# Optimization experiments

Hardware: AMD Instinct MI355X
Metric: run time of the kernel (lower is better)

## Reference

```python
import jax, jax.numpy as jnp
import numpy as np

N_ATOMS = 200_000
N_EDGES = 10_000_000
N_MOL = 128


def setup_inputs() -> dict:
    key = jax.random.key(0)
    k1, k2, k3, k4, k5, k6, k7 = jax.random.split(key, 7)
    dEdRij = jax.random.normal(k1, (N_EDGES, 3), dtype=jnp.float32)
    Rij = jax.random.normal(k2, (N_EDGES, 3), dtype=jnp.float32)
    R = jax.random.normal(k3, (N_ATOMS, 3), dtype=jnp.float32)
    # Non-degenerate cells: ~10 Angstrom cubic boxes with small perturbation
    cell = jnp.eye(3, dtype=jnp.float32) * 10.0 + 0.1 * jax.random.normal(k4, (N_MOL, 3, 3), dtype=jnp.float32)
    idx_i = jax.random.randint(k5, (N_EDGES,), 0, N_ATOMS, dtype=jnp.int32)
    idx_j = jax.random.randint(k6, (N_EDGES,), 0, N_ATOMS, dtype=jnp.int32)
    idx_m = jnp.sort(jax.random.randint(k7, (N_ATOMS,), 0, N_MOL, dtype=jnp.int32))
    return {"dEdRij": dEdRij, "Rij": Rij, "R": R, "cell": cell,
            "idx_i": idx_i, "idx_j": idx_j, "idx_m": idx_m}


def reference(dEdRij, Rij, R, cell, idx_i, idx_j, idx_m):
    N = R.shape[0]
    M = cell.shape[0]
    # Forces: F = sum_{edges into i} dE/dRij - sum_{edges from j} dE/dRij
    forces = jnp.zeros_like(R).at[idx_i].add(dEdRij).at[idx_j].add(-dEdRij)
    # Per-edge outer product [E,3,3]: Rij[:, :, None] * dEdRij[:, None, :]
    stress_edge = dEdRij[:, None, :] * Rij[:, :, None]
    # Scatter to atoms, then reduce atoms -> molecules
    stress_i = jnp.zeros((N, 3, 3), dtype=R.dtype).at[idx_i].add(stress_edge)
    stress = jax.ops.segment_sum(stress_i, idx_m, num_segments=M)  # [M,3,3]
    # Cell volume via scalar triple product a . (b x c)
    volume = jnp.sum(cell[:, 0, :] * jnp.cross(cell[:, 1, :], cell[:, 2, :]), axis=1)  # [M]
    stress_out = (stress / volume[:, None, None]).reshape(M * 3, 3)
    return forces, stress_out
```

## Files before the change

### kernel.cpp

```cpp
#include <hip/hip_runtime.h>
#include <hip/hip_bf16.h>
#include <hip/hip_fp16.h>

#define N_MOL 128
#define STRESS_FLOATS (N_MOL * 9)
#define NB 128
#define APB 1563
#define NPAD (NB * APB)
#define EPB 1024
#define K_PT 4
#define BLK 256
#define RS_SLICES 16
#define STRESS_BLOCKS 2048

__global__ void zero_i32_kernel(int* __restrict__ p, int n) {
    int i = blockIdx.x * blockDim.x + threadIdx.x;
    if (i < n) p[i] = 0;
}

__device__ __forceinline__ unsigned short h16(float v) {
    return __half_as_ushort(__float2half_rn(v));
}

__global__ void __launch_bounds__(256)
stress_kernel(const float* __restrict__ dEdRij,
              const float* __restrict__ Rij,
              const int*   __restrict__ idx_i,
              const int*   __restrict__ idx_m,
              float* __restrict__ spart,
              int E)
{
    __shared__ float smem[STRESS_FLOATS];
    for (int t = threadIdx.x; t < STRESS_FLOATS; t += blockDim.x) smem[t] = 0.f;
    __syncthreads();

    const int stride = gridDim.x * blockDim.x;
    for (int e = blockIdx.x * blockDim.x + threadIdx.x; e < E; e += stride) {
        const int i = idx_i[e];
        const int m = idx_m[i];
        const float dx = dEdRij[3*e+0], dy = dEdRij[3*e+1], dz = dEdRij[3*e+2];
        const float rx = Rij[3*e+0],    ry = Rij[3*e+1],    rz = Rij[3*e+2];
        float* s = &smem[m * 9];
        atomicAdd(&s[0], rx * dx);
        atomicAdd(&s[1], rx * dy);
        atomicAdd(&s[2], rx * dz);
        atomicAdd(&s[3], ry * dx);
        atomicAdd(&s[4], ry * dy);
        atomicAdd(&s[5], ry * dz);
        atomicAdd(&s[6], rz * dx);
        atomicAdd(&s[7], rz * dy);
        atomicAdd(&s[8], rz * dz);
    }

    __syncthreads();
    float* sp = spart + (size_t)blockIdx.x * STRESS_FLOATS;
    for (int t = threadIdx.x; t < STRESS_FLOATS; t += blockDim.x)
        sp[t] = smem[t];
}

__global__ void __launch_bounds__(256)
scatter_kernel(const float* __restrict__ dEdRij,
               const int*   __restrict__ idx_i,
               const int*   __restrict__ idx_j,
               uint2* __restrict__ rec,
               int*   __restrict__ cnt,
               int e0_chunk, int n_edges_chunk, int CAP)
{
    __shared__ int           hist[NB];
    __shared__ int           excl[NB];
    __shared__ int           cur[NB];
    __shared__ int           shiftb[NB];
    __shared__ uint2         stg[EPB * 2];
    __shared__ unsigned char stgb[EPB * 2];

    for (int t = threadIdx.x; t < NB; t += blockDim.x) hist[t] = 0;
    __syncthreads();

    const int be0 = e0_chunk + blockIdx.x * EPB;
    const int be1 = min(be0 + EPB, e0_chunk + n_edges_chunk);

    int ei[K_PT], ej[K_PT];
    #pragma unroll
    for (int k = 0; k < K_PT; ++k) {
        const int e = be0 + k * BLK + threadIdx.x;
        ei[k] = -1; ej[k] = -1;
        if (e < be1) {
            ei[k] = idx_i[e];
            ej[k] = idx_j[e];
            atomicAdd(&hist[ei[k] / APB], 1);
            atomicAdd(&hist[ej[k] / APB], 1);
        }
    }
    __syncthreads();

    if (threadIdx.x < 64) {
        const int l = threadIdx.x;
        const int a = hist[2 * l], b = hist[2 * l + 1];
        int s = a + b;
        #pragma unroll
        for (int off = 1; off < 64; off <<= 1) {
            const int v = __shfl_up(s, off, 64);
            if (l >= off) s += v;
        }
        const int excl_pair = s - (a + b);
        excl[2 * l]     = excl_pair;
        excl[2 * l + 1] = excl_pair + a;
    }
    __syncthreads();

    for (int t = threadIdx.x; t < NB; t += blockDim.x) {
        const int h  = hist[t];
        const int ex = excl[t];
        const int g  = h ? atomicAdd(&cnt[t], h) : 0;
        cur[t]    = ex;
        shiftb[t] = t * CAP + g - ex;
    }
    __syncthreads();

    #pragma unroll
    for (int k = 0; k < K_PT; ++k) {
        const int e = be0 + k * BLK + threadIdx.x;
        if (e >= be1) continue;
        const int i = ei[k], j = ej[k];
        const float dx = dEdRij[3*e+0], dy = dEdRij[3*e+1], dz = dEdRij[3*e+2];

        const int bi = i / APB;
        const int li = i - bi * APB;
        uint2 q;
        q.x = ((unsigned)li << 16) | h16(dx);
        q.y = (unsigned)h16(dy) | ((unsigned)h16(dz) << 16);
        int p = atomicAdd(&cur[bi], 1);
        stg[p] = q; stgb[p] = (unsigned char)bi;

        const int bj = j / APB;
        const int lj = j - bj * APB;
        q.x = ((unsigned)lj << 16) | h16(-dx);
        q.y = (unsigned)h16(-dy) | ((unsigned)h16(-dz) << 16);
        p = atomicAdd(&cur[bj], 1);
        stg[p] = q; stgb[p] = (unsigned char)bj;
    }
    __syncthreads();

    const int total = 2 * (be1 - be0);
    for (int t = threadIdx.x; t < total; t += blockDim.x) {
        const int b = stgb[t];
        const int gidx = t + shiftb[b];
        if (gidx < (b + 1) * CAP)
            rec[gidx] = stg[t];
    }
}

__global__ void __launch_bounds__(256)
accum_kernel(const uint2* __restrict__ rec,
             const int*   __restrict__ cnt,
             float* __restrict__ partial,
             int CAP, int S, int store)
{
    __shared__ float facc[APB * 3];
    const int b = blockIdx.x / S;
    const int s = blockIdx.x - b * S;
    for (int t = threadIdx.x; t < APB * 3; t += blockDim.x) facc[t] = 0.f;
    __syncthreads();

    int n = cnt[b];
    if (n > CAP) n = CAP;
    int r0 = (int)((long long)n * s / S);
    int r1 = (int)((long long)n * (s + 1) / S);
    const uint2* rb = rec + (size_t)b * CAP;

#define ACC1(w0, w1)                                                  \
    {                                                                 \
        const int   l  = (int)((w0) >> 16);                           \
        const float fx = __half2float(__ushort_as_half(               \
                             (unsigned short)((w0) & 0xffffu)));      \
        const float fy = __half2float(__ushort_as_half(               \
                             (unsigned short)((w1) & 0xffffu)));      \
        const float fz = __half2float(__ushort_as_half(               \
                             (unsigned short)((w1) >> 16)));          \
        atomicAdd(&facc[l * 3 + 0], fx);                              \
        atomicAdd(&facc[l * 3 + 1], fy);                              \
        atomicAdd(&facc[l * 3 + 2], fz);                              \
    }

    if (r0 < r1 && (r0 & 1)) {
        if (threadIdx.x == 0) { const uint2 q = rb[r0]; ACC1(q.x, q.y); }
        ++r0;
    }
    if (r0 < r1 && (r1 & 1)) {
        --r1;
        if (threadIdx.x == 0) { const uint2 q = rb[r1]; ACC1(q.x, q.y); }
    }
    const int npair = (r1 - r0) >> 1;
    const uint4* rp = (const uint4*)(rb + r0);

    int p = threadIdx.x;
    for (; p + 7 * BLK < npair; p += 8 * BLK) {
        uint4 q0 = rp[p];
        uint4 q1 = rp[p + 1 * BLK];
        uint4 q2 = rp[p + 2 * BLK];
        uint4 q3 = rp[p + 3 * BLK];
        uint4 q4 = rp[p + 4 * BLK];
        uint4 q5 = rp[p + 5 * BLK];
        uint4 q6 = rp[p + 6 * BLK];
        uint4 q7 = rp[p + 7 * BLK];
        ACC1(q0.x, q0.y); ACC1(q0.z, q0.w);
        ACC1(q1.x, q1.y); ACC1(q1.z, q1.w);
        ACC1(q2.x, q2.y); ACC1(q2.z, q2.w);
        ACC1(q3.x, q3.y); ACC1(q3.z, q3.w);
        ACC1(q4.x, q4.y); ACC1(q4.z, q4.w);
        ACC1(q5.x, q5.y); ACC1(q5.z, q5.w);
        ACC1(q6.x, q6.y); ACC1(q6.z, q6.w);
        ACC1(q7.x, q7.y); ACC1(q7.z, q7.w);
    }
    for (; p < npair; p += BLK) {
        const uint4 q = rp[p];
        ACC1(q.x, q.y); ACC1(q.z, q.w);
    }
#undef ACC1

    __syncthreads();
    float* pp = partial + ((size_t)s * NPAD + (size_t)b * APB) * 3;
    if (store) {
        for (int t = threadIdx.x; t < APB * 3; t += blockDim.x)
            pp[t] = facc[t];
    } else {
        for (int t = threadIdx.x; t < APB * 3; t += blockDim.x)
            pp[t] += facc[t];
    }
}

__global__ void final_forces_kernel(const float* __restrict__ partial,
                                    float* __restrict__ forces, int n3, int S)
{
    const int t = blockIdx.x * blockDim.x + threadIdx.x;
    if (t >= n3) return;
    float a = 0.f;
    for (int s = 0; s < S; ++s)
        a += partial[(size_t)s * NPAD * 3 + t];
    forces[t] = a;
}

__global__ void reduce_stress_stage1(const float* __restrict__ spart,
                                     float* __restrict__ stmp, int rows)
{
    const int t = blockIdx.x * blockDim.x + threadIdx.x;
    if (t >= STRESS_FLOATS * RS_SLICES) return;
    const int col = t % STRESS_FLOATS;
    const int sl  = t / STRESS_FLOATS;
    float acc = 0.f;
    for (int r = sl; r < rows; r += RS_SLICES)
        acc += spart[(size_t)r * STRESS_FLOATS + col];
    stmp[sl * STRESS_FLOATS + col] = acc;
}

__global__ void reduce_stress_stage2(const float* __restrict__ stmp,
                                     const float* __restrict__ cell,
                                     float* __restrict__ out_stress)
{
    const int t = blockIdx.x * blockDim.x + threadIdx.x;
    if (t >= STRESS_FLOATS) return;
    float acc = 0.f;
    #pragma unroll
    for (int s = 0; s < RS_SLICES; ++s)
        acc += stmp[s * STRESS_FLOATS + t];
    const int m = t / 9;
    const float* c = &cell[m * 9];
    const float a0 = c[0], a1 = c[1], a2 = c[2];
    const float b0 = c[3], b1 = c[4], b2 = c[5];
    const float c0 = c[6], c1 = c[7], c2 = c[8];
    const float x0 = b1 * c2 - b2 * c1;
    const float x1 = b2 * c0 - b0 * c2;
    const float x2 = b0 * c1 - b1 * c0;
    const float vol = a0 * x0 + a1 * x1 + a2 * x2;
    out_stress[t] = acc / vol;
}

__global__ void zero_f64_kernel(double* __restrict__ p, int n) {
    int i = blockIdx.x * blockDim.x + threadIdx.x;
    if (i < n) p[i] = 0.0;
}

__global__ void __launch_bounds__(256)
edge_kernel_f64(const float* __restrict__ dEdRij,
                const float* __restrict__ Rij,
                const int*   __restrict__ idx_i,
                const int*   __restrict__ idx_j,
                const int*   __restrict__ idx_m,
                double* __restrict__ facc,
                float*  __restrict__ spart,
                int E)
{
    __shared__ float smem[STRESS_FLOATS];
    for (int t = threadIdx.x; t < STRESS_FLOATS; t += blockDim.x) smem[t] = 0.f;
    __syncthreads();
    const int stride = gridDim.x * blockDim.x;
    for (int e = blockIdx.x * blockDim.x + threadIdx.x; e < E; e += stride) {
        const int i = idx_i[e], j = idx_j[e];
        const float dx = dEdRij[3*e+0], dy = dEdRij[3*e+1], dz = dEdRij[3*e+2];
        const float rx = Rij[3*e+0],    ry = Rij[3*e+1],    rz = Rij[3*e+2];
        double* fi = facc + 3 * (size_t)i;
        unsafeAtomicAdd(fi + 0, (double) dx);
        unsafeAtomicAdd(fi + 1, (double) dy);
        unsafeAtomicAdd(fi + 2, (double) dz);
        double* fj = facc + 3 * (size_t)j;
        unsafeAtomicAdd(fj + 0, (double)-dx);
        unsafeAtomicAdd(fj + 1, (double)-dy);
        unsafeAtomicAdd(fj + 2, (double)-dz);
        const int m = idx_m[i];
        float* s = &smem[m * 9];
        atomicAdd(&s[0], rx*dx); atomicAdd(&s[1], rx*dy); atomicAdd(&s[2], rx*dz);
        atomicAdd(&s[3], ry*dx); atomicAdd(&s[4], ry*dy); atomicAdd(&s[5], ry*dz);
        atomicAdd(&s[6], rz*dx); atomicAdd(&s[7], rz*dy); atomicAdd(&s[8], rz*dz);
    }
    __syncthreads();
    float* sp = spart + (size_t)blockIdx.x * STRESS_FLOATS;
    for (int t = threadIdx.x; t < STRESS_FLOATS; t += blockDim.x) sp[t] = smem[t];
}

__global__ void reduce_forces_f64_kernel(const double* __restrict__ facc,
                                         float* __restrict__ forces, int n3)
{
    int t = blockIdx.x * blockDim.x + threadIdx.x;
    if (t < n3) forces[t] = (float)facc[t];
}

extern "C" void kernel_launch(void* const* d_in, const int* in_sizes, int n_in,
                              void* d_out, int out_size, void* d_ws, size_t ws_size,
                              hipStream_t stream)
{
    const float* dEdRij = (const float*)d_in[0];
    const float* Rij    = (const float*)d_in[1];
    const float* R      = (const float*)d_in[2];  (void)R;
    const float* cell   = (const float*)d_in[3];
    const int*   idx_i  = (const int*)d_in[4];
    const int*   idx_j  = (const int*)d_in[5];
    const int*   idx_m  = (const int*)d_in[6];

    const int E  = in_sizes[0] / 3;
    const int N  = in_sizes[2] / 3;
    const int n3 = N * 3;

    float* out        = (float*)d_out;
    float* forces     = out;
    float* stress_out = out + (size_t)n3;

    int nchunks = 0, SEG = 0, CAP = 0;
    size_t rec_u2 = 0;
    const size_t spart_f = (size_t)STRESS_BLOCKS * STRESS_FLOATS;
    {
        const int cand[14][2] = {
            {2,16},{2,8},{3,16},{3,8},{2,4},{4,8},{4,4},{2,2},
            {5,4},{8,4},{10,2},{16,2},{20,2},{40,1}};
        for (int ci = 0; ci < 14; ++ci) {
            const int nc = cand[ci][0];
            const int S  = cand[ci][1];
            const int CH = (E + nc - 1) / nc;
            const long long mean = 2LL * CH / NB;
            int cap = (int)(mean + mean / 8 + 64);
            cap = (cap + 1) & ~1;
            const size_t need = (size_t)NB * cap * sizeof(uint2)
                              + spart_f * sizeof(float)
                              + (size_t)nc * NB * sizeof(int)
                              + (size_t)RS_SLICES * STRESS_FLOATS * sizeof(float)
                              + (size_t)S * NPAD * 3 * sizeof(float)
                              + 256;
            if (need <= ws_size) {
                nchunks = nc; SEG = S; CAP = cap;
                rec_u2  = (size_t)NB * cap;
                break;
            }
        }
    }

    if (nchunks > 0) {
        uint2* rec   = (uint2*)d_ws;
        float* spart = (float*)(rec + rec_u2);
        int*   cnt   = (int*)(spart + spart_f);
        float* stmp  = (float*)(cnt + (size_t)nchunks * NB);
        float* part  = stmp + (size_t)RS_SLICES * STRESS_FLOATS;

        zero_i32_kernel<<<(nchunks * NB + BLK - 1) / BLK, BLK, 0, stream>>>(
            cnt, nchunks * NB);

        stress_kernel<<<STRESS_BLOCKS, BLK, 0, stream>>>(
            dEdRij, Rij, idx_i, idx_m, spart, E);

        const int CH = (E + nchunks - 1) / nchunks;
        int chunk = 0;
        for (int s = 0; s < E; s += CH, ++chunk) {
            const int ce = min(CH, E - s);
            const int nb = (ce + EPB - 1) / EPB;

            scatter_kernel<<<nb, BLK, 0, stream>>>(
                dEdRij, idx_i, idx_j,
                rec, cnt + (size_t)chunk * NB, s, ce, CAP);

            accum_kernel<<<NB * SEG, BLK, 0, stream>>>(
                rec, cnt + (size_t)chunk * NB, part, CAP, SEG,
                chunk == 0 ? 1 : 0);
        }

        final_forces_kernel<<<(n3 + BLK - 1) / BLK, BLK, 0, stream>>>(
            part, forces, n3, SEG);
        reduce_stress_stage1<<<(STRESS_FLOATS * RS_SLICES + BLK - 1) / BLK,
                               BLK, 0, stream>>>(spart, stmp, STRESS_BLOCKS);
        reduce_stress_stage2<<<(STRESS_FLOATS + BLK - 1) / BLK, BLK, 0, stream>>>(
            stmp, cell, stress_out);
    } else {
        double* facc   = (double*)d_ws;
        float*  spartf = (float*)(facc + n3);

        zero_f64_kernel<<<(n3 + BLK - 1) / BLK, BLK, 0, stream>>>(facc, n3);
        edge_kernel_f64<<<2048, BLK, 0, stream>>>(
            dEdRij, Rij, idx_i, idx_j, idx_m, facc, spartf, E);
        reduce_forces_f64_kernel<<<(n3 + BLK - 1) / BLK, BLK, 0, stream>>>(
            facc, forces, n3);
        reduce_stress_stage1<<<(STRESS_FLOATS * RS_SLICES + BLK - 1) / BLK,
                               BLK, 0, stream>>>(spartf, (float*)(spartf + (size_t)2048 * STRESS_FLOATS), 2048);
        reduce_stress_stage2<<<(STRESS_FLOATS + BLK - 1) / BLK, BLK, 0, stream>>>(
            (float*)(spartf + (size_t)2048 * STRESS_FLOATS), cell, stress_out);
    }
}
```

Measured before the change: 1.066 ms.

## Fuse stress accumulation into scatter kernel to avoid second pass over edges

The separate stress kernel is removed. The per-edge outer-product stress accumulation now happens inside the scatter kernel, reusing the dEdRij and idx_i loads already done there. Each scatter block adds its shared-memory stress into a per-block row across chunks, with one row per block and a combined zeroing kernel. This saves a full re-read of dEdRij and idx_i, but adds shared-memory atomics and LDS pressure to the scatter kernel and raises the stress-reduction slice count. The candidate list, SEG options and capacity slack are also retuned.

```diff
diff --git a/kernel.cpp b/kernel.cpp
--- a/kernel.cpp
+++ b/kernel.cpp
@@ -10,12 +10,11 @@
 #define EPB 1024
 #define K_PT 4
 #define BLK 256
-#define RS_SLICES 16
-#define STRESS_BLOCKS 2048
-
-__global__ void zero_i32_kernel(int* __restrict__ p, int n) {
-    int i = blockIdx.x * blockDim.x + threadIdx.x;
-    if (i < n) p[i] = 0;
+#define RS_SLICES 64
+
+__global__ void zero_f32_kernel(float* __restrict__ p, size_t n) {
+    size_t i = (size_t)blockIdx.x * blockDim.x + threadIdx.x;
+    if (i < n) p[i] = 0.f;
 }
 
 __device__ __forceinline__ unsigned short h16(float v) {
@@ -23,57 +22,26 @@
 }
 
 __global__ void __launch_bounds__(256)
-stress_kernel(const float* __restrict__ dEdRij,
-              const float* __restrict__ Rij,
-              const int*   __restrict__ idx_i,
-              const int*   __restrict__ idx_m,
-              float* __restrict__ spart,
-              int E)
-{
-    __shared__ float smem[STRESS_FLOATS];
-    for (int t = threadIdx.x; t < STRESS_FLOATS; t += blockDim.x) smem[t] = 0.f;
-    __syncthreads();
-
-    const int stride = gridDim.x * blockDim.x;
-    for (int e = blockIdx.x * blockDim.x + threadIdx.x; e < E; e += stride) {
-        const int i = idx_i[e];
-        const int m = idx_m[i];
-        const float dx = dEdRij[3*e+0], dy = dEdRij[3*e+1], dz = dEdRij[3*e+2];
-        const float rx = Rij[3*e+0],    ry = Rij[3*e+1],    rz = Rij[3*e+2];
-        float* s = &smem[m * 9];
-        atomicAdd(&s[0], rx * dx);
-        atomicAdd(&s[1], rx * dy);
-        atomicAdd(&s[2], rx * dz);
-        atomicAdd(&s[3], ry * dx);
-        atomicAdd(&s[4], ry * dy);
-        atomicAdd(&s[5], ry * dz);
-        atomicAdd(&s[6], rz * dx);
-        atomicAdd(&s[7], rz * dy);
-        atomicAdd(&s[8], rz * dz);
-    }
-
-    __syncthreads();
-    float* sp = spart + (size_t)blockIdx.x * STRESS_FLOATS;
-    for (int t = threadIdx.x; t < STRESS_FLOATS; t += blockDim.x)
-        sp[t] = smem[t];
-}
-
-__global__ void __launch_bounds__(256)
 scatter_kernel(const float* __restrict__ dEdRij,
+               const float* __restrict__ Rij,
                const int*   __restrict__ idx_i,
                const int*   __restrict__ idx_j,
+               const int*   __restrict__ idx_m,
                uint2* __restrict__ rec,
                int*   __restrict__ cnt,
+               float* __restrict__ spart,
                int e0_chunk, int n_edges_chunk, int CAP)
 {
     __shared__ int           hist[NB];
     __shared__ int           excl[NB];
     __shared__ int           cur[NB];
     __shared__ int           shiftb[NB];
+    __shared__ float         smem[STRESS_FLOATS];
     __shared__ uint2         stg[EPB * 2];
     __shared__ unsigned char stgb[EPB * 2];
 
     for (int t = threadIdx.x; t < NB; t += blockDim.x) hist[t] = 0;
+    for (int t = threadIdx.x; t < STRESS_FLOATS; t += blockDim.x) smem[t] = 0.f;
     __syncthreads();
 
     const int be0 = e0_chunk + blockIdx.x * EPB;
@@ -123,6 +91,19 @@
         if (e >= be1) continue;
         const int i = ei[k], j = ej[k];
         const float dx = dEdRij[3*e+0], dy = dEdRij[3*e+1], dz = dEdRij[3*e+2];
+        const float rx = Rij[3*e+0],    ry = Rij[3*e+1],    rz = Rij[3*e+2];
+
+        const int m = idx_m[i];
+        float* s = &smem[m * 9];
+        atomicAdd(&s[0], rx * dx);
+        atomicAdd(&s[1], rx * dy);
+        atomicAdd(&s[2], rx * dz);
+        atomicAdd(&s[3], ry * dx);
+        atomicAdd(&s[4], ry * dy);
+        atomicAdd(&s[5], ry * dz);
+        atomicAdd(&s[6], rz * dx);
+        atomicAdd(&s[7], rz * dy);
+        atomicAdd(&s[8], rz * dz);
 
         const int bi = i / APB;
         const int li = i - bi * APB;
@@ -148,6 +129,11 @@
         if (gidx < (b + 1) * CAP)
             rec[gidx] = stg[t];
     }
+
+    __syncthreads();
+    float* sp = spart + (size_t)blockIdx.x * STRESS_FLOATS;
+    for (int t = threadIdx.x; t < STRESS_FLOATS; t += blockDim.x)
+        sp[t] += smem[t];
 }
 
 __global__ void __launch_bounds__(256)
@@ -260,7 +246,6 @@
     const int t = blockIdx.x * blockDim.x + threadIdx.x;
     if (t >= STRESS_FLOATS) return;
     float acc = 0.f;
-    #pragma unroll
     for (int s = 0; s < RS_SLICES; ++s)
         acc += stmp[s * STRESS_FLOATS + t];
     const int m = t / 9;
@@ -344,29 +329,30 @@
     float* forces     = out;
     float* stress_out = out + (size_t)n3;
 
-    int nchunks = 0, SEG = 0, CAP = 0;
-    size_t rec_u2 = 0;
-    const size_t spart_f = (size_t)STRESS_BLOCKS * STRESS_FLOATS;
+    int nchunks = 0, SEG = 0, CAP = 0, ROWS = 0;
+    size_t rec_u2 = 0, spart_f = 0;
     {
         const int cand[14][2] = {
-            {2,16},{2,8},{3,16},{3,8},{2,4},{4,8},{4,4},{2,2},
-            {5,4},{8,4},{10,2},{16,2},{20,2},{40,1}};
+            {2,8},{2,4},{3,8},{3,4},{4,8},{4,4},{2,2},{5,4},
+            {8,4},{8,2},{10,2},{16,2},{20,2},{40,1}};
         for (int ci = 0; ci < 14; ++ci) {
             const int nc = cand[ci][0];
             const int S  = cand[ci][1];
             const int CH = (E + nc - 1) / nc;
             const long long mean = 2LL * CH / NB;
-            int cap = (int)(mean + mean / 8 + 64);
+            int cap = (int)(mean + mean / 16 + 64);
             cap = (cap + 1) & ~1;
+            const int rows = (CH + EPB - 1) / EPB;
             const size_t need = (size_t)NB * cap * sizeof(uint2)
-                              + spart_f * sizeof(float)
+                              + (size_t)rows * STRESS_FLOATS * sizeof(float)
                               + (size_t)nc * NB * sizeof(int)
                               + (size_t)RS_SLICES * STRESS_FLOATS * sizeof(float)
                               + (size_t)S * NPAD * 3 * sizeof(float)
                               + 256;
             if (need <= ws_size) {
-                nchunks = nc; SEG = S; CAP = cap;
+                nchunks = nc; SEG = S; CAP = cap; ROWS = rows;
                 rec_u2  = (size_t)NB * cap;
+                spart_f = (size_t)rows * STRESS_FLOATS;
                 break;
             }
         }
@@ -379,11 +365,9 @@
         float* stmp  = (float*)(cnt + (size_t)nchunks * NB);
         float* part  = stmp + (size_t)RS_SLICES * STRESS_FLOATS;
 
-        zero_i32_kernel<<<(nchunks * NB + BLK - 1) / BLK, BLK, 0, stream>>>(
-            cnt, nchunks * NB);
-
-        stress_kernel<<<STRESS_BLOCKS, BLK, 0, stream>>>(
-            dEdRij, Rij, idx_i, idx_m, spart, E);
+        const size_t zf = spart_f + (size_t)nchunks * NB;
+        zero_f32_kernel<<<(int)((zf + BLK - 1) / BLK), BLK, 0, stream>>>(
+            spart, zf);
 
         const int CH = (E + nchunks - 1) / nchunks;
         int chunk = 0;
@@ -392,8 +376,8 @@
             const int nb = (ce + EPB - 1) / EPB;
 
             scatter_kernel<<<nb, BLK, 0, stream>>>(
-                dEdRij, idx_i, idx_j,
-                rec, cnt + (size_t)chunk * NB, s, ce, CAP);
+                dEdRij, Rij, idx_i, idx_j, idx_m,
+                rec, cnt + (size_t)chunk * NB, spart, s, ce, CAP);
 
             accum_kernel<<<NB * SEG, BLK, 0, stream>>>(
                 rec, cnt + (size_t)chunk * NB, part, CAP, SEG,
@@ -403,7 +387,7 @@
         final_forces_kernel<<<(n3 + BLK - 1) / BLK, BLK, 0, stream>>>(
             part, forces, n3, SEG);
         reduce_stress_stage1<<<(STRESS_FLOATS * RS_SLICES + BLK - 1) / BLK,
-                               BLK, 0, stream>>>(spart, stmp, STRESS_BLOCKS);
+                               BLK, 0, stream>>>(spart, stmp, ROWS);
         reduce_stress_stage2<<<(STRESS_FLOATS + BLK - 1) / BLK, BLK, 0, stream>>>(
             stmp, cell, stress_out);
     } else {
@@ -416,7 +400,8 @@
         reduce_forces_f64_kernel<<<(n3 + BLK - 1) / BLK, BLK, 0, stream>>>(
             facc, forces, n3);
         reduce_stress_stage1<<<(STRESS_FLOATS * RS_SLICES + BLK - 1) / BLK,
-                               BLK, 0, stream>>>(spartf, (float*)(spartf + (size_t)2048 * STRESS_FLOATS), 2048);
+                               BLK, 0, stream>>>(
+            spartf, (float*)(spartf + (size_t)2048 * STRESS_FLOATS), 2048);
         reduce_stress_stage2<<<(STRESS_FLOATS + BLK - 1) / BLK, BLK, 0, stream>>>(
             (float*)(spartf + (size_t)2048 * STRESS_FLOATS), cell, stress_out);
     }
```

New measurement: 945.0 us. 11.3% less time.
